# Performance work log

Hardware: AMD Instinct MI355X
Metric: run time of the kernel (lower is better)

The kernel has to match this reference:

```python
import jax, jax.numpy as jnp
import numpy as np

N_NODES = 50000
N_EDGES = 800000
D_IN = 788
D_HID = 256
N_REL = 7
N_CLS = 2


def rgcn_conv(x, w_rel, w_root, b, src, dst, edge_type):
    """PyG RGCNConv with default mean aggregation per relation + root weight + bias.
    x: (N, F_in); w_rel: (R, F_in, F_out); w_root: (F_in, F_out); b: (F_out,).
    src/dst: (E,) with edge_index[0]=source j, edge_index[1]=target i.
    """
    R, _, F_out = w_rel.shape
    N = x.shape[0]
    # transform-then-gather (equivalent to PyG's gather-then-transform, cheaper)
    x_rel = jnp.einsum('nf,rfo->rno', x, w_rel)          # (R, N, F_out)
    msg = x_rel[edge_type, src]                           # (E, F_out)
    agg = jnp.zeros((R, N, F_out), x.dtype).at[edge_type, dst].add(msg)
    cnt = jnp.zeros((R, N), x.dtype).at[edge_type, dst].add(1.0)
    out = (agg / jnp.clip(cnt, 1.0)[..., None]).sum(0)    # mean per relation, summed over relations
    return out + x @ w_root + b


def setup_inputs() -> dict:
    key = jax.random.key(0)
    ks = jax.random.split(key, 9)
    x = jax.random.normal(ks[0], (N_NODES, D_IN), dtype=jnp.float32)
    edge_index = jax.random.randint(ks[1], (2, N_EDGES), 0, N_NODES, dtype=jnp.int64)
    edge_type = jax.random.randint(ks[2], (N_EDGES,), 0, N_REL, dtype=jnp.int64)
    s1 = 0.05
    w1_rel = jax.random.normal(ks[3], (N_REL, D_IN, D_HID), dtype=jnp.float32) * s1
    w1_root = jax.random.normal(ks[4], (D_IN, D_HID), dtype=jnp.float32) * s1
    b1 = jnp.zeros((D_HID,), dtype=jnp.float32)
    w2_rel = jax.random.normal(ks[5], (N_REL, D_HID, N_CLS), dtype=jnp.float32) * s1
    w2_root = jax.random.normal(ks[6], (D_HID, N_CLS), dtype=jnp.float32) * s1
    b2 = jnp.zeros((N_CLS,), dtype=jnp.float32)
    return {"x": x, "edge_index": edge_index, "edge_type": edge_type,
            "w1_rel": w1_rel, "w1_root": w1_root, "b1": b1,
            "w2_rel": w2_rel, "w2_root": w2_root, "b2": b2}


def reference(x, edge_index, edge_type, w1_rel, w1_root, b1, w2_rel, w2_root, b2):
    src, dst = edge_index[0], edge_index[1]
    h = jax.nn.relu(rgcn_conv(x, w1_rel, w1_root, b1, src, dst, edge_type))
    # F.dropout(p=0.5) is identity in eval mode
    out = rgcn_conv(h, w2_rel, w2_root, b2, src, dst, edge_type)
    return out
```

## Files before the change

kernel.cpp:

```cpp
#include <hip/hip_runtime.h>
#include <hip/hip_bf16.h>
#include <stdint.h>

#define N_NODES 50000
#define N_EDGES 800000
#define D_IN    788
#define D_INP   800
#define D_HID   256
#define N_REL   7
#define NBINS   (N_REL * N_NODES)
#define NSCANB  342

typedef __attribute__((ext_vector_type(8))) short bf16x8;
typedef __attribute__((ext_vector_type(4))) float f32x4;
typedef __attribute__((ext_vector_type(4))) unsigned int u32x4;

__device__ __forceinline__ unsigned short f2bf(float f) {
  union { __hip_bfloat16 h; unsigned short u; } v;
  v.h = __float2bfloat16(f);
  return v.u;
}

__device__ __forceinline__ f32x4 bf4(ushort4 g) {
  union { unsigned int u; float f; } a, b, c, d;
  a.u = (unsigned)g.x << 16; b.u = (unsigned)g.y << 16;
  c.u = (unsigned)g.z << 16; d.u = (unsigned)g.w << 16;
  return (f32x4){a.f, b.f, c.f, d.f};
}

#define GLOAD16(g, l) __builtin_amdgcn_global_load_lds(                      \
    (const __attribute__((address_space(1))) unsigned int*)(g),              \
    (__attribute__((address_space(3))) unsigned int*)(l), 16, 0, 0)

__global__ void k_conv_w(const float* __restrict__ w_rel, const float* __restrict__ w_root,
                         unsigned short* __restrict__ wt) {
  int t = blockIdx.x * blockDim.x + threadIdx.x;
  if (t >= 8 * D_HID * 100) return;
  int m = t / (D_HID * 100);
  int rem = t % (D_HID * 100);
  int o = rem / 100, gi = rem % 100;
  int chunk = gi >> 2, p = gi & 3;
  int g = p ^ ((o >> 1) & 3);
  int k0 = chunk * 32 + g * 8;
  const float* src = (m < N_REL) ? (w_rel + (size_t)m * D_IN * D_HID) : w_root;
  union { unsigned short us[8]; u32x4 v; } pk;
#pragma unroll
  for (int j = 0; j < 8; j++)
    pk.us[j] = (k0 + j < D_IN) ? f2bf(src[(size_t)(k0 + j) * D_HID + o]) : (unsigned short)0;
  *(u32x4*)(wt + (size_t)(m * D_HID + o) * D_INP + chunk * 32 + p * 8) = pk.v;
}

__global__ void k_xbf(const float* __restrict__ x, unsigned short* __restrict__ xb) {
  int t = blockIdx.x * blockDim.x + threadIdx.x;
  if (t >= N_NODES * 100) return;
  int n = t / 100, gi = t % 100;
  int chunk = gi >> 2, p = gi & 3;
  int g = p ^ ((n >> 1) & 3);
  int c = chunk * 32 + g * 8;
  union { unsigned short us[8]; u32x4 v; } pk;
  if (c + 7 < D_IN) {
    float4 a = *(const float4*)(x + (size_t)n * D_IN + c);
    float4 b = *(const float4*)(x + (size_t)n * D_IN + c + 4);
    pk.us[0] = f2bf(a.x); pk.us[1] = f2bf(a.y); pk.us[2] = f2bf(a.z); pk.us[3] = f2bf(a.w);
    pk.us[4] = f2bf(b.x); pk.us[5] = f2bf(b.y); pk.us[6] = f2bf(b.z); pk.us[7] = f2bf(b.w);
  } else {
#pragma unroll
    for (int j = 0; j < 8; j++)
      pk.us[j] = (c + j < D_IN) ? f2bf(x[(size_t)n * D_IN + c + j]) : (unsigned short)0;
  }
  *(u32x4*)(xb + (size_t)n * D_INP + chunk * 32 + p * 8) = pk.v;
}

__global__ void k_count(const int* __restrict__ etype, const int* __restrict__ edst,
                        int* __restrict__ cnt) {
  int t = blockIdx.x * blockDim.x + threadIdx.x;
  if (t >= N_EDGES) return;
  atomicAdd(&cnt[etype[t] * N_NODES + edst[t]], 1);
}

__global__ void k_scan1(const int* __restrict__ cnt, int* __restrict__ bsum) {
  __shared__ int wsh[4];
  int b = blockIdx.x, tid = threadIdx.x;
  int base = b * 1024 + tid * 4;
  int4 v = {0, 0, 0, 0};
  if (base + 3 < NBINS) v = *(const int4*)(cnt + base);
  else { for (int i = 0; i < 4; i++) if (base + i < NBINS) ((int*)&v)[i] = cnt[base + i]; }
  int s = v.x + v.y + v.z + v.w;
  for (int o = 32; o > 0; o >>= 1) s += __shfl_down(s, o);
  if ((tid & 63) == 0) wsh[tid >> 6] = s;
  __syncthreads();
  if (tid == 0) bsum[b] = wsh[0] + wsh[1] + wsh[2] + wsh[3];
}

__global__ void k_scan2(const int* __restrict__ bsum, int* __restrict__ boff) {
  __shared__ int tmp[512];
  int tid = threadIdx.x;
  int mine = (tid < NSCANB) ? bsum[tid] : 0;
  tmp[tid] = mine;
  __syncthreads();
  for (int o = 1; o < 512; o <<= 1) {
    int v = (tid >= o) ? tmp[tid - o] : 0;
    __syncthreads();
    tmp[tid] += v;
    __syncthreads();
  }
  if (tid < NSCANB) boff[tid] = tmp[tid] - mine;
}

__global__ void k_scan3(const int* __restrict__ cnt, const int* __restrict__ boff,
                        int* __restrict__ S) {
  __shared__ int wsum[4];
  int b = blockIdx.x, tid = threadIdx.x;
  int base = b * 1024 + tid * 4;
  int4 v = {0, 0, 0, 0};
  if (base + 3 < NBINS) v = *(const int4*)(cnt + base);
  else { for (int i = 0; i < 4; i++) if (base + i < NBINS) ((int*)&v)[i] = cnt[base + i]; }
  int s = v.x + v.y + v.z + v.w;
  int lane = tid & 63, w = tid >> 6;
  int sc = s;
  for (int o = 1; o < 64; o <<= 1) { int u = __shfl_up(sc, o); if (lane >= o) sc += u; }
  if (lane == 63) wsum[w] = sc;
  __syncthreads();
  int wbase = 0;
  for (int i = 0; i < w; i++) wbase += wsum[i];
  int excl = boff[b] + wbase + sc - s;
  int o0 = excl, o1 = excl + v.x, o2 = o1 + v.y, o3 = o2 + v.z;
  if (base + 3 < NBINS) { int4 o4 = {o0, o1, o2, o3}; *(int4*)(S + base) = o4; }
  else {
    if (base     < NBINS) S[base]     = o0;
    if (base + 1 < NBINS) S[base + 1] = o1;
    if (base + 2 < NBINS) S[base + 2] = o2;
    if (base + 3 < NBINS) S[base + 3] = o3;
  }
}

__global__ void k_scatter(const int* __restrict__ etype, const int* __restrict__ edst,
                          const int* __restrict__ esrc, const int* __restrict__ S,
                          int* __restrict__ rank, int* __restrict__ psrc) {
  int t = blockIdx.x * blockDim.x + threadIdx.x;
  if (t >= N_EDGES) return;
  int bin = etype[t] * N_NODES + edst[t];
  int r = atomicAdd(&rank[bin], 1);
  psrc[S[bin] + r] = esrc[t];
}

__global__ __launch_bounds__(512) void k_gemm_g(
    const unsigned short* __restrict__ xb, const unsigned short* __restrict__ wt,
    unsigned short* __restrict__ xrs, int mb) {
  __shared__ __align__(16) unsigned short As[128 * 32];
  __shared__ __align__(16) unsigned short Bs[256 * 32];

  int tid = threadIdx.x;
  int mat = mb + blockIdx.y;
  int m0 = blockIdx.x * 128;
  const unsigned short* wsec = wt + (size_t)mat * (D_HID * D_INP);
  int lane = tid & 63, w = tid >> 6;
  int wm = w >> 2, wn = w & 3;

  int ar = tid >> 2;
  int arow = m0 + ar; if (arow > N_NODES - 1) arow = N_NODES - 1;
  const unsigned short* asrc = xb + (size_t)arow * D_INP + (tid & 3) * 8;
  const unsigned short* bsrc0 = wsec + (size_t)(tid >> 2) * D_INP + (tid & 3) * 8;
  const unsigned short* bsrc1 = bsrc0 + (size_t)128 * D_INP;
  unsigned short* al = As + tid * 8;
  unsigned short* bl0 = Bs + tid * 8;
  unsigned short* bl1 = Bs + 4096 + tid * 8;

  f32x4 acc[4][4];
#pragma unroll
  for (int i = 0; i < 4; i++)
#pragma unroll
    for (int j = 0; j < 4; j++) acc[i][j] = (f32x4){0.f, 0.f, 0.f, 0.f};

  int row = lane & 15, quad = lane >> 4;
  int rg = (quad ^ ((row >> 1) & 3)) * 8;

  for (int ks = 0; ks < 25; ks++) {
    int ko = ks * 32;
    GLOAD16(asrc + ko, al);
    GLOAD16(bsrc0 + ko, bl0);
    GLOAD16(bsrc1 + ko, bl1);
    __syncthreads();

    bf16x8 af[4], bfr[4];
#pragma unroll
    for (int i = 0; i < 4; i++)
      af[i] = *(const bf16x8*)(As + (wm * 64 + i * 16 + row) * 32 + rg);
#pragma unroll
    for (int j = 0; j < 4; j++)
      bfr[j] = *(const bf16x8*)(Bs + (wn * 64 + j * 16 + row) * 32 + rg);
#pragma unroll
    for (int i = 0; i < 4; i++)
#pragma unroll
      for (int j = 0; j < 4; j++)
        acc[i][j] = __builtin_amdgcn_mfma_f32_16x16x32_bf16(af[i], bfr[j], acc[i][j], 0, 0, 0);
    __syncthreads();
  }

  int col_l = lane & 15, rquad = lane >> 4;
  unsigned short* xo = xrs + (size_t)blockIdx.y * ((size_t)N_NODES * D_HID);
#pragma unroll
  for (int i = 0; i < 4; i++) {
#pragma unroll
    for (int reg = 0; reg < 4; reg++) {
      int node = m0 + wm * 64 + i * 16 + rquad * 4 + reg;
      if (node < N_NODES) {
#pragma unroll
        for (int j = 0; j < 4; j++)
          xo[(size_t)node * D_HID + wn * 64 + j * 16 + col_l] = f2bf(acc[i][j][reg]);
      }
    }
  }
}

__global__ __launch_bounds__(256) void k_gemm_f(
    const float* __restrict__ x, const unsigned short* __restrict__ wt,
    unsigned short* __restrict__ xrs, int mb) {
  __shared__ __align__(16) unsigned short As[64 * 40];
  __shared__ __align__(16) unsigned short Bs[256 * 40];

  int tid = threadIdx.x;
  int mat = mb + blockIdx.y;
  int m0 = blockIdx.x * 64;
  const unsigned short* wsec = wt + (size_t)mat * (D_HID * D_INP);
  int lane = tid & 63, w = tid >> 6;

  int ra = tid >> 2, ca = tid & 3, ca8 = ca * 8;
  int arow = m0 + ra; if (arow > N_NODES - 1) arow = N_NODES - 1;
  const float* apf = x + (size_t)arow * D_IN;
  const unsigned short* bgp = wsec + (size_t)ra * D_INP + (ca ^ ((ra >> 1) & 3)) * 8;
  unsigned short* al = As + ra * 40 + ca8;
  unsigned short* bl = Bs + ra * 40 + ca8;

  f32x4 acc[4][4];
#pragma unroll
  for (int i = 0; i < 4; i++)
#pragma unroll
    for (int j = 0; j < 4; j++) acc[i][j] = (f32x4){0.f, 0.f, 0.f, 0.f};

  float4 pa0 = *(const float4*)(apf + ca8);
  float4 pa1 = *(const float4*)(apf + ca8 + 4);
  u32x4 pb0 = *(const u32x4*)(bgp);
  u32x4 pb1 = *(const u32x4*)(bgp +  64 * D_INP);
  u32x4 pb2 = *(const u32x4*)(bgp + 128 * D_INP);
  u32x4 pb3 = *(const u32x4*)(bgp + 192 * D_INP);

  int row = lane & 15, quad = lane >> 4;
  for (int ks = 0; ks < 25; ks++) {
    if (ks < 24) {
      union { unsigned short us[8]; u32x4 v; } pk;
      pk.us[0] = f2bf(pa0.x); pk.us[1] = f2bf(pa0.y);
      pk.us[2] = f2bf(pa0.z); pk.us[3] = f2bf(pa0.w);
      pk.us[4] = f2bf(pa1.x); pk.us[5] = f2bf(pa1.y);
      pk.us[6] = f2bf(pa1.z); pk.us[7] = f2bf(pa1.w);
      *(u32x4*)al = pk.v;
    } else {
      float v0 = pa0.x, v1 = pa0.y, v2 = pa0.z, v3 = pa0.w;
      float v4 = pa1.x, v5 = pa1.y, v6 = pa1.z, v7 = pa1.w;
      if (ca8 == 16) { v0 = pa1.x; v1 = pa1.y; v2 = pa1.z; v3 = pa1.w;
                       v4 = 0.f; v5 = 0.f; v6 = 0.f; v7 = 0.f; }
      if (ca8 == 24) { v0 = 0.f; v1 = 0.f; v2 = 0.f; v3 = 0.f;
                       v4 = 0.f; v5 = 0.f; v6 = 0.f; v7 = 0.f; }
      union { unsigned short us[8]; u32x4 v; } pk;
      pk.us[0] = f2bf(v0); pk.us[1] = f2bf(v1); pk.us[2] = f2bf(v2); pk.us[3] = f2bf(v3);
      pk.us[4] = f2bf(v4); pk.us[5] = f2bf(v5); pk.us[6] = f2bf(v6); pk.us[7] = f2bf(v7);
      *(u32x4*)al = pk.v;
    }
    *(u32x4*)bl = pb0;
    *(u32x4*)(bl +  64 * 40) = pb1;
    *(u32x4*)(bl + 128 * 40) = pb2;
    *(u32x4*)(bl + 192 * 40) = pb3;
    __syncthreads();

    if (ks < 24) {
      int on = (ks + 1) * 32 + ca8;
      int lo = (on > 780) ? 780 : on;
      pa0 = *(const float4*)(apf + lo);
      pa1 = *(const float4*)(apf + lo + 4);
      int ko = (ks + 1) * 32;
      pb0 = *(const u32x4*)(bgp + ko);
      pb1 = *(const u32x4*)(bgp + ko +  64 * D_INP);
      pb2 = *(const u32x4*)(bgp + ko + 128 * D_INP);
      pb3 = *(const u32x4*)(bgp + ko + 192 * D_INP);
    }

    bf16x8 af[4], bfr[4];
#pragma unroll
    for (int i = 0; i < 4; i++)
      af[i] = *(const bf16x8*)(As + (i * 16 + row) * 40 + quad * 8);
#pragma unroll
    for (int j = 0; j < 4; j++)
      bfr[j] = *(const bf16x8*)(Bs + (w * 64 + j * 16 + row) * 40 + quad * 8);
#pragma unroll
    for (int i = 0; i < 4; i++)
#pragma unroll
      for (int j = 0; j < 4; j++)
        acc[i][j] = __builtin_amdgcn_mfma_f32_16x16x32_bf16(af[i], bfr[j], acc[i][j], 0, 0, 0);
    __syncthreads();
  }

  int col_l = lane & 15, rquad = lane >> 4;
  unsigned short* xo = xrs + (size_t)blockIdx.y * ((size_t)N_NODES * D_HID);
#pragma unroll
  for (int i = 0; i < 4; i++) {
#pragma unroll
    for (int reg = 0; reg < 4; reg++) {
      int node = m0 + i * 16 + rquad * 4 + reg;
      if (node < N_NODES) {
#pragma unroll
        for (int j = 0; j < 4; j++)
          xo[(size_t)node * D_HID + w * 64 + j * 16 + col_l] = f2bf(acc[i][j][reg]);
      }
    }
  }
}

__global__ __launch_bounds__(256) void k_agg(
    const unsigned short* __restrict__ xrs, const int* __restrict__ S,
    const int* __restrict__ cnt, const int* __restrict__ psrc,
    float* __restrict__ h, const float* __restrict__ b1,
    const float* __restrict__ w2rel, const float* __restrict__ w2root,
    float* __restrict__ y, int r0, int pass) {
  int n = blockIdx.x * 4 + (threadIdx.x >> 6);
  int lane = threadIdx.x & 63;
  if (n >= N_NODES) return;
  f32x4 acc;
  if (pass == 0) acc = (f32x4){0.f, 0.f, 0.f, 0.f};
  else acc = *(const f32x4*)(h + (size_t)n * D_HID + lane * 4);

  int nr = (pass < 3) ? 2 : 1;
  for (int rr = 0; rr < nr; rr++) {
    int bin = (r0 + rr) * N_NODES + n;
    int c = cnt[bin];
    if (c > 0) {
      int p = S[bin];
      f32x4 s = (f32x4){0.f, 0.f, 0.f, 0.f};
      int e = 0;
      for (; e + 1 < c; e += 2) {
        int s0 = psrc[p + e], s1 = psrc[p + e + 1];
        ushort4 g0 = *(const ushort4*)(xrs + ((size_t)rr * N_NODES + s0) * D_HID + lane * 4);
        ushort4 g1 = *(const ushort4*)(xrs + ((size_t)rr * N_NODES + s1) * D_HID + lane * 4);
        s += bf4(g0) + bf4(g1);
      }
      if (e < c) {
        int s0 = psrc[p + e];
        ushort4 g0 = *(const ushort4*)(xrs + ((size_t)rr * N_NODES + s0) * D_HID + lane * 4);
        s += bf4(g0);
      }
      acc += s * (1.0f / (float)c);
    }
  }

  if (pass < 3) {
    *(f32x4*)(h + (size_t)n * D_HID + lane * 4) = acc;
    return;
  }

  ushort4 gr = *(const ushort4*)(xrs + ((size_t)1 * N_NODES + n) * D_HID + lane * 4);
  acc += bf4(gr);
  f32x4 b = *(const f32x4*)(b1 + lane * 4);
  f32x4 hv;
  hv[0] = fmaxf(acc[0] + b[0], 0.f);
  hv[1] = fmaxf(acc[1] + b[1], 0.f);
  hv[2] = fmaxf(acc[2] + b[2], 0.f);
  hv[3] = fmaxf(acc[3] + b[3], 0.f);

#pragma unroll
  for (int m = 0; m < 8; m++) {
    const float* wp = (m < N_REL) ? (w2rel + m * (D_HID * 2)) : w2root;
    f32x4 wa = *(const f32x4*)(wp + lane * 8);
    f32x4 wb = *(const f32x4*)(wp + lane * 8 + 4);
    float d0 = hv[0] * wa[0] + hv[1] * wa[2] + hv[2] * wb[0] + hv[3] * wb[2];
    float d1 = hv[0] * wa[1] + hv[1] * wa[3] + hv[2] * wb[1] + hv[3] * wb[3];
#pragma unroll
    for (int off = 32; off > 0; off >>= 1) {
      d0 += __shfl_down(d0, off);
      d1 += __shfl_down(d1, off);
    }
    if (lane == 0) {
      y[(size_t)m * (N_NODES * 2) + n * 2]     = d0;
      y[(size_t)m * (N_NODES * 2) + n * 2 + 1] = d1;
    }
  }
}

__global__ void k_out(const float* __restrict__ y, const float* __restrict__ b2,
                      const int* __restrict__ cnt, const int* __restrict__ S,
                      const int* __restrict__ psrc, float* __restrict__ out) {
  int t = blockIdx.x * blockDim.x + threadIdx.x;
  if (t < NBINS) {
    int c = cnt[t];
    if (c == 0) return;
    int p = S[t];
    int r = t / N_NODES;
    int i = t - r * N_NODES;
    const float* yr = y + (size_t)r * (N_NODES * 2);
    float s0 = 0.f, s1 = 0.f;
    for (int e = 0; e < c; e++) {
      int sc = psrc[p + e];
      float2 v = *(const float2*)(yr + sc * 2);
      s0 += v.x; s1 += v.y;
    }
    float is = 1.0f / (float)c;
    atomicAdd(out + (size_t)i * 2,     s0 * is);
    atomicAdd(out + (size_t)i * 2 + 1, s1 * is);
  } else if (t < NBINS + N_NODES) {
    int i = t - NBINS;
    float2 v = *(const float2*)(y + (size_t)N_REL * (N_NODES * 2) + i * 2);
    atomicAdd(out + (size_t)i * 2,     v.x + b2[0]);
    atomicAdd(out + (size_t)i * 2 + 1, v.y + b2[1]);
  }
}

#define OFF_WT   0u
#define OFF_XRS  3276800u
#define OFF_H    54476800u
#define OFF_CNT  105676800u
#define OFF_RANK 107076800u
#define OFF_S    108476800u
#define OFF_PSRC 109876800u
#define OFF_Y    113076800u
#define OFF_BSUM 116276800u
#define OFF_BOFF 116278848u
#define OFF_XB   116280896u
#define WS_NEED_XB 196280896ull

extern "C" void kernel_launch(void* const* d_in, const int* in_sizes, int n_in,
                              void* d_out, int out_size, void* d_ws, size_t ws_size,
                              hipStream_t stream) {
  const float* x      = (const float*)d_in[0];
  const int*   eidx   = (const int*)d_in[1];
  const int*   etype  = (const int*)d_in[2];
  const float* w1rel  = (const float*)d_in[3];
  const float* w1root = (const float*)d_in[4];
  const float* b1     = (const float*)d_in[5];
  const float* w2rel  = (const float*)d_in[6];
  const float* w2root = (const float*)d_in[7];
  const float* b2     = (const float*)d_in[8];
  float* out = (float*)d_out;
  char* ws = (char*)d_ws;

  unsigned short* wt  = (unsigned short*)(ws + OFF_WT);
  unsigned short* xrs = (unsigned short*)(ws + OFF_XRS);
  float* h    = (float*)(ws + OFF_H);
  int*   cnt  = (int*)(ws + OFF_CNT);
  int*   rank = (int*)(ws + OFF_RANK);
  int*   S    = (int*)(ws + OFF_S);
  int*   psrc = (int*)(ws + OFF_PSRC);
  float* y    = (float*)(ws + OFF_Y);
  int*   bsum = (int*)(ws + OFF_BSUM);
  int*   boff = (int*)(ws + OFF_BOFF);
  unsigned short* xb = (unsigned short*)(ws + OFF_XB);
  const int* esrc = eidx;
  const int* edst = eidx + N_EDGES;

  const bool big = (ws_size >= WS_NEED_XB);

  hipMemsetAsync(ws + OFF_CNT, 0, 2800000u, stream);
  hipMemsetAsync(d_out, 0, (size_t)out_size * sizeof(float), stream);

  k_conv_w<<<(8 * D_HID * 100 + 255) / 256, 256, 0, stream>>>(w1rel, w1root, wt);
  if (big)
    k_xbf<<<(N_NODES * 100 + 255) / 256, 256, 0, stream>>>(x, xb);
  k_count<<<(N_EDGES + 255) / 256, 256, 0, stream>>>(etype, edst, cnt);
  k_scan1<<<NSCANB, 256, 0, stream>>>(cnt, bsum);
  k_scan2<<<1, 512, 0, stream>>>(bsum, boff);
  k_scan3<<<NSCANB, 256, 0, stream>>>(cnt, boff, S);
  k_scatter<<<(N_EDGES + 255) / 256, 256, 0, stream>>>(etype, edst, esrc, S, rank, psrc);

  for (int p = 0; p < 4; p++) {
    if (big)
      k_gemm_g<<<dim3((N_NODES + 127) / 128, 2), 512, 0, stream>>>(xb, wt, xrs, 2 * p);
    else
      k_gemm_f<<<dim3(782, 2), 256, 0, stream>>>(x, wt, xrs, 2 * p);
    k_agg<<<(N_NODES + 3) / 4, 256, 0, stream>>>(xrs, S, cnt, psrc, h,
                                                 b1, w2rel, w2root, y, 2 * p, p);
  }

  k_out<<<(NBINS + N_NODES + 255) / 256, 256, 0, stream>>>(y, b2, cnt, S, psrc, out);
}
```

Before: 793.3 us.

## Add full-workspace path: single 8-matrix GEMM launch and one-pass aggregation

When the workspace is large enough, all eight transformed feature slabs (seven relations plus root) are computed in one swizzled GEMM launch, replacing four paired launches. A new aggregation kernel then sums all relations per node in a single pass, applying bias, ReLU and the layer-2 projection, so the fp32 hidden buffer is never written and reread across passes. The swizzled block order is meant to improve cache reuse of the weight and input tiles. The cost is roughly 100 MB of extra workspace, and this path only runs if the harness provides it.

```diff
diff --git a/kernel.cpp b/kernel.cpp
--- a/kernel.cpp
+++ b/kernel.cpp
@@ -10,6 +10,7 @@
 #define N_REL   7
 #define NBINS   (N_REL * N_NODES)
 #define NSCANB  342
+#define NXTILE  391
 
 typedef __attribute__((ext_vector_type(8))) short bf16x8;
 typedef __attribute__((ext_vector_type(4))) float f32x4;
@@ -144,6 +145,7 @@
   psrc[S[bin] + r] = esrc[t];
 }
 
+template<int SWZ, int NMAT>
 __global__ __launch_bounds__(512) void k_gemm_g(
     const unsigned short* __restrict__ xb, const unsigned short* __restrict__ wt,
     unsigned short* __restrict__ xrs, int mb) {
@@ -151,8 +153,16 @@
   __shared__ __align__(16) unsigned short Bs[256 * 32];
 
   int tid = threadIdx.x;
-  int mat = mb + blockIdx.y;
-  int m0 = blockIdx.x * 128;
+  int bx, by;
+  if (SWZ) {
+    int b = blockIdx.x;
+    int l = (b % 8) * (NXTILE * NMAT / 8) + b / 8;
+    bx = l / NMAT; by = l % NMAT;
+  } else {
+    bx = blockIdx.x; by = blockIdx.y;
+  }
+  int mat = mb + by;
+  int m0 = bx * 128;
   const unsigned short* wsec = wt + (size_t)mat * (D_HID * D_INP);
   int lane = tid & 63, w = tid >> 6;
   int wm = w >> 2, wn = w & 3;
@@ -198,7 +208,7 @@
   }
 
   int col_l = lane & 15, rquad = lane >> 4;
-  unsigned short* xo = xrs + (size_t)blockIdx.y * ((size_t)N_NODES * D_HID);
+  unsigned short* xo = xrs + (size_t)by * ((size_t)N_NODES * D_HID);
 #pragma unroll
   for (int i = 0; i < 4; i++) {
 #pragma unroll
@@ -315,6 +325,73 @@
   }
 }
 
+__global__ __launch_bounds__(256) void k_agg8(
+    const unsigned short* __restrict__ xrs, const int* __restrict__ S,
+    const int* __restrict__ cnt, const int* __restrict__ psrc,
+    const float* __restrict__ b1, const float* __restrict__ w2rel,
+    const float* __restrict__ w2root, float* __restrict__ y) {
+  int n = blockIdx.x * 4 + (threadIdx.x >> 6);
+  int lane = threadIdx.x & 63;
+  if (n >= N_NODES) return;
+
+  int c_l = 0, p_l = 0;
+  if (lane < N_REL) {
+    c_l = cnt[lane * N_NODES + n];
+    p_l = S[lane * N_NODES + n];
+  }
+
+  f32x4 acc = (f32x4){0.f, 0.f, 0.f, 0.f};
+#pragma unroll
+  for (int r = 0; r < N_REL; r++) {
+    int c = __shfl(c_l, r);
+    if (c > 0) {
+      int p = __shfl(p_l, r);
+      const unsigned short* slab = xrs + (size_t)r * N_NODES * D_HID;
+      f32x4 s = (f32x4){0.f, 0.f, 0.f, 0.f};
+      int e = 0;
+      for (; e + 1 < c; e += 2) {
+        int s0 = psrc[p + e], s1 = psrc[p + e + 1];
+        ushort4 g0 = *(const ushort4*)(slab + (size_t)s0 * D_HID + lane * 4);
+        ushort4 g1 = *(const ushort4*)(slab + (size_t)s1 * D_HID + lane * 4);
+        s += bf4(g0) + bf4(g1);
+      }
+      if (e < c) {
+        int s0 = psrc[p + e];
+        ushort4 g0 = *(const ushort4*)(slab + (size_t)s0 * D_HID + lane * 4);
+        s += bf4(g0);
+      }
+      acc += s * (1.0f / (float)c);
+    }
+  }
+
+  ushort4 gr = *(const ushort4*)(xrs + ((size_t)7 * N_NODES + n) * D_HID + lane * 4);
+  acc += bf4(gr);
+  f32x4 b = *(const f32x4*)(b1 + lane * 4);
+  f32x4 hv;
+  hv[0] = fmaxf(acc[0] + b[0], 0.f);
+  hv[1] = fmaxf(acc[1] + b[1], 0.f);
+  hv[2] = fmaxf(acc[2] + b[2], 0.f);
+  hv[3] = fmaxf(acc[3] + b[3], 0.f);
+
+#pragma unroll
+  for (int m = 0; m < 8; m++) {
+    const float* wp = (m < N_REL) ? (w2rel + m * (D_HID * 2)) : w2root;
+    f32x4 wa = *(const f32x4*)(wp + lane * 8);
+    f32x4 wb = *(const f32x4*)(wp + lane * 8 + 4);
+    float d0 = hv[0] * wa[0] + hv[1] * wa[2] + hv[2] * wb[0] + hv[3] * wb[2];
+    float d1 = hv[0] * wa[1] + hv[1] * wa[3] + hv[2] * wb[1] + hv[3] * wb[3];
+#pragma unroll
+    for (int off = 32; off > 0; off >>= 1) {
+      d0 += __shfl_down(d0, off);
+      d1 += __shfl_down(d1, off);
+    }
+    if (lane == 0) {
+      y[(size_t)m * (N_NODES * 2) + n * 2]     = d0;
+      y[(size_t)m * (N_NODES * 2) + n * 2 + 1] = d1;
+    }
+  }
+}
+
 __global__ __launch_bounds__(256) void k_agg(
     const unsigned short* __restrict__ xrs, const int* __restrict__ S,
     const int* __restrict__ cnt, const int* __restrict__ psrc,
@@ -425,6 +502,18 @@
 #define OFF_XB   116280896u
 #define WS_NEED_XB 196280896ull
 
+#define F_OFF_WT   0u
+#define F_OFF_XRS  3276800u
+#define F_OFF_CNT  208076800u
+#define F_OFF_RANK 209476800u
+#define F_OFF_S    210876800u
+#define F_OFF_PSRC 212276800u
+#define F_OFF_Y    215476800u
+#define F_OFF_BSUM 218676800u
+#define F_OFF_BOFF 218678848u
+#define F_OFF_XB   218680896u
+#define WS_NEED_FULL 298680896ull
+
 extern "C" void kernel_launch(void* const* d_in, const int* in_sizes, int n_in,
                               void* d_out, int out_size, void* d_ws, size_t ws_size,
                               hipStream_t stream) {
@@ -439,6 +528,42 @@
   const float* b2     = (const float*)d_in[8];
   float* out = (float*)d_out;
   char* ws = (char*)d_ws;
+  const int* esrc = eidx;
+  const int* edst = eidx + N_EDGES;
+
+  const bool full = (ws_size >= WS_NEED_FULL);
+  const bool big  = !full && (ws_size >= WS_NEED_XB);
+
+  hipMemsetAsync(d_out, 0, (size_t)out_size * sizeof(float), stream);
+
+  if (full) {
+    unsigned short* wt  = (unsigned short*)(ws + F_OFF_WT);
+    unsigned short* xrs = (unsigned short*)(ws + F_OFF_XRS);
+    int*   cnt  = (int*)(ws + F_OFF_CNT);
+    int*   rank = (int*)(ws + F_OFF_RANK);
+    int*   S    = (int*)(ws + F_OFF_S);
+    int*   psrc = (int*)(ws + F_OFF_PSRC);
+    float* y    = (float*)(ws + F_OFF_Y);
+    int*   bsum = (int*)(ws + F_OFF_BSUM);
+    int*   boff = (int*)(ws + F_OFF_BOFF);
+    unsigned short* xb = (unsigned short*)(ws + F_OFF_XB);
+
+    hipMemsetAsync(ws + F_OFF_CNT, 0, 2800000u, stream);
+
+    k_conv_w<<<(8 * D_HID * 100 + 255) / 256, 256, 0, stream>>>(w1rel, w1root, wt);
+    k_xbf<<<(N_NODES * 100 + 255) / 256, 256, 0, stream>>>(x, xb);
+    k_count<<<(N_EDGES + 255) / 256, 256, 0, stream>>>(etype, edst, cnt);
+    k_scan1<<<NSCANB, 256, 0, stream>>>(cnt, bsum);
+    k_scan2<<<1, 512, 0, stream>>>(bsum, boff);
+    k_scan3<<<NSCANB, 256, 0, stream>>>(cnt, boff, S);
+    k_scatter<<<(N_EDGES + 255) / 256, 256, 0, stream>>>(etype, edst, esrc, S, rank, psrc);
+
+    k_gemm_g<1, 8><<<NXTILE * 8, 512, 0, stream>>>(xb, wt, xrs, 0);
+    k_agg8<<<(N_NODES + 3) / 4, 256, 0, stream>>>(xrs, S, cnt, psrc,
+                                                  b1, w2rel, w2root, y);
+    k_out<<<(NBINS + N_NODES + 255) / 256, 256, 0, stream>>>(y, b2, cnt, S, psrc, out);
+    return;
+  }
 
   unsigned short* wt  = (unsigned short*)(ws + OFF_WT);
   unsigned short* xrs = (unsigned short*)(ws + OFF_XRS);
@@ -451,13 +576,8 @@
   int*   bsum = (int*)(ws + OFF_BSUM);
   int*   boff = (int*)(ws + OFF_BOFF);
   unsigned short* xb = (unsigned short*)(ws + OFF_XB);
-  const int* esrc = eidx;
-  const int* edst = eidx + N_EDGES;
-
-  const bool big = (ws_size >= WS_NEED_XB);
 
   hipMemsetAsync(ws + OFF_CNT, 0, 2800000u, stream);
-  hipMemsetAsync(d_out, 0, (size_t)out_size * sizeof(float), stream);
 
   k_conv_w<<<(8 * D_HID * 100 + 255) / 256, 256, 0, stream>>>(w1rel, w1root, wt);
   if (big)
@@ -470,7 +590,7 @@
 
   for (int p = 0; p < 4; p++) {
     if (big)
-      k_gemm_g<<<dim3((N_NODES + 127) / 128, 2), 512, 0, stream>>>(xb, wt, xrs, 2 * p);
+      k_gemm_g<0, 2><<<dim3(NXTILE, 2), 512, 0, stream>>>(xb, wt, xrs, 2 * p);
     else
       k_gemm_f<<<dim3(782, 2), 256, 0, stream>>>(x, wt, xrs, 2 * p);
     k_agg<<<(N_NODES + 3) / 4, 256, 0, stream>>>(xrs, S, cnt, psrc, h,
```

New measurement: 723.6 us. -8.8%, faster.
